# Kernel tuning notes

Measured on AMD Instinct MI355X. Metric: run time of the kernel, lower is better.

The kernel has to match this reference:

```python
import jax, jax.numpy as jnp
import numpy as np
from jax import lax

T, B, D = 1024, 32, 1024


def setup_inputs() -> dict:
    key = jax.random.key(0)
    k1, k2, k3, k4 = jax.random.split(key, 4)
    xav = (6.0 / (D + D)) ** 0.5  # xavier_uniform bound
    return {
        "x": jax.random.normal(k1, (T, B, D), dtype=jnp.float32),
        "h0": jnp.zeros((B, D), dtype=jnp.float32),
        "W_alpha": jax.random.uniform(k2, (D, D), minval=-xav, maxval=xav, dtype=jnp.float32),
        "d_alpha": jnp.full((D,), 0.1, dtype=jnp.float32),
        "b_alpha": jnp.full((D,), 2.0, dtype=jnp.float32),
        "W_x": jax.random.uniform(k3, (D, D), minval=-xav, maxval=xav, dtype=jnp.float32),
        "b_v": jnp.zeros((D,), dtype=jnp.float32),
    }


def reference(x, h0, W_alpha, d_alpha, b_alpha, W_x, b_v):
    # Precompute batched GEMMs once (x_t @ W.T), as in the original.
    alpha_x = jnp.einsum("tbd,ed->tbe", x, W_alpha)          # [T,B,D]
    v = jnp.tanh(jnp.einsum("tbd,ed->tbe", x, W_x) + b_v)    # [T,B,D]

    def step(h_prev, inp):
        ax_t, v_t = inp
        alpha = jax.nn.sigmoid(ax_t + d_alpha * h_prev + b_alpha)
        h_new = alpha * h_prev + (1.0 - alpha) * v_t
        out = h_new * h_new * jax.nn.sigmoid(h_new)  # h * silu(h)
        return h_new, (h_new, out)

    _, (hs, outs) = lax.scan(step, h0, (alpha_x, v))
    h = jnp.concatenate([h0[None], hs], axis=0)  # [T+1,B,D]
    return outs, h
```

## Files before the change

kernel.cpp:

```cpp
#include <hip/hip_runtime.h>
#include <hip/hip_bf16.h>
#include <stdint.h>

#define TT 1024
#define BB 32
#define DD 1024
#define MROWS (TT*BB)
#define NCOLS (2*DD)
#define KDIM  (DD)
#define SS (BB*DD)

typedef __attribute__((ext_vector_type(8))) short short8;
typedef __attribute__((ext_vector_type(4))) float f32x4;

__device__ __forceinline__ float bf2f(uint16_t u){
  union { uint32_t u; float f; } c; c.u = ((uint32_t)u) << 16; return c.f;
}
__device__ __forceinline__ uint16_t f2bf(float f){
  union { float f; uint32_t u; } c; c.f = f;
  uint32_t u = c.u;
  u += 0x7FFFu + ((u >> 16) & 1u);
  return (uint16_t)(u >> 16);
}
__device__ __forceinline__ float tanh_fast(float x){
  return 1.f - 2.f/(1.f + __expf(2.f*x));
}
__device__ __forceinline__ float sigmoid_fast(float x){
  return __builtin_amdgcn_rcpf(1.f + __expf(-x));
}

__global__ __launch_bounds__(256) void cvt_x_kernel(const float* __restrict__ x,
                                                    uint16_t* __restrict__ xb, int n4){
  int i = blockIdx.x * 256 + threadIdx.x;
  int stride = gridDim.x * 256;
  for (; i < n4; i += stride){
    float4 f = ((const float4*)x)[i];
    ushort4 o;
    o.x = f2bf(f.x); o.y = f2bf(f.y); o.z = f2bf(f.z); o.w = f2bf(f.w);
    ((ushort4*)xb)[i] = o;
  }
}

__global__ __launch_bounds__(256) void cvt_w_kernel(const float* __restrict__ Wa,
                                                    const float* __restrict__ Wx,
                                                    uint16_t* __restrict__ wc){
  int i = blockIdx.x * 256 + threadIdx.x;
  const int c    = i >> 8;
  const int col4 = i & 255;
  const int e = ((c >> 5) << 4) | (c & 15);
  const int s = (c >> 4) & 1;
  const float* src = (s ? Wx : Wa) + (size_t)e*DD + col4*4;
  float4 f = *(const float4*)src;
  ushort4 o;
  o.x = f2bf(f.x); o.y = f2bf(f.y); o.z = f2bf(f.z); o.w = f2bf(f.w);
  ((ushort4*)wc)[i] = o;
}

__global__ __launch_bounds__(512, 2) void gemm_dual(const uint16_t* __restrict__ xb,
                                                    const uint16_t* __restrict__ wc,
                                                    const float* __restrict__ bv,
                                                    uint32_t* __restrict__ av){
  __shared__ __align__(16) uint16_t lds[65536];
  char* ldsc = (char*)lds;

  const int tid  = threadIdx.x;
  const int lane = tid & 63;
  const int w    = tid >> 6;
  const int wm   = w >> 2;
  const int wn   = w & 3;
  const int fr   = lane & 15;
  const int fq   = lane >> 4;

  const int bid = blockIdx.x;
  const int bsw = (bid & 7) * 128 + (bid >> 3);
  const int bm  = (bsw >> 3) << 8;
  const int bn  = (bsw & 7) << 8;

  f32x4 acc[8][4] = {};

  const int srow = tid >> 3;
  const int soff = ((tid & 7) ^ (srow & 7)) * 8;

  #define STAGE(kt, q) { \
    const uint16_t* src_ = ((q) < 2) ? xb : wc; \
    const int gbase_ = ((q) < 2) ? bm : bn; \
    const int region_ = ((q) < 2) ? 0 : 65536; \
    const int rb0_ = ((q) & 1) * 128; \
    const int k0_ = (kt) * 64; \
    _Pragma("unroll") \
    for (int c_ = 0; c_ < 2; ++c_){ \
      const uint16_t* g_ = src_ + (size_t)(gbase_ + rb0_ + c_*64 + srow)*KDIM + k0_ + soff; \
      char* d_ = ldsc + region_ + ((kt) & 1)*32768 + (rb0_ + c_*64 + w*8)*128; \
      __builtin_amdgcn_global_load_lds((const __attribute__((address_space(1))) void*)g_, \
                                       (__attribute__((address_space(3))) void*)d_, 16, 0, 0); \
    } \
  }

  STAGE(0,0) STAGE(0,1) STAGE(0,2) STAGE(0,3)
  asm volatile("s_waitcnt vmcnt(0)" ::: "memory");
  __builtin_amdgcn_s_barrier();

  for (int t = 0; t < 16; ++t){
    const int nbuf = (t & 1) * 32768;
    const int aB0 = nbuf + (wm*128 + fr)*128;
    const int bB0 = 65536 + nbuf + (wn*64 + fr)*128;
    int aK[2], bK[2];
    #pragma unroll
    for (int kh = 0; kh < 2; ++kh){
      const int ps = ((kh*4 + fq) ^ (fr & 7)) * 16;
      aK[kh] = aB0 + ps;
      bK[kh] = bB0 + ps;
    }

    #define PHASE(q) { \
      short8 aF[4][2], bF[2][2]; \
      _Pragma("unroll") \
      for (int m = 0; m < 4; ++m) \
        _Pragma("unroll") \
        for (int kh = 0; kh < 2; ++kh) \
          aF[m][kh] = *(const short8*)(ldsc + aK[kh] + (((q)&1)*8192 + m*2048)); \
      _Pragma("unroll") \
      for (int n = 0; n < 2; ++n) \
        _Pragma("unroll") \
        for (int kh = 0; kh < 2; ++kh) \
          bF[n][kh] = *(const short8*)(ldsc + bK[kh] + (((q)>>1)*4096 + n*2048)); \
      if (t < 15) STAGE(t+1, q) \
      __builtin_amdgcn_s_barrier(); \
      asm volatile("s_waitcnt lgkmcnt(0)" ::: "memory"); \
      __builtin_amdgcn_sched_barrier(0); \
      __builtin_amdgcn_s_setprio(1); \
      _Pragma("unroll") \
      for (int m = 0; m < 4; ++m) \
        _Pragma("unroll") \
        for (int n = 0; n < 2; ++n) \
          _Pragma("unroll") \
          for (int kh = 0; kh < 2; ++kh) \
            acc[((q)&1)*4+m][((q)>>1)*2+n] = \
              __builtin_amdgcn_mfma_f32_16x16x32_bf16(aF[m][kh], bF[n][kh], \
                                                      acc[((q)&1)*4+m][((q)>>1)*2+n], 0, 0, 0); \
      __builtin_amdgcn_s_setprio(0); \
      if ((q) == 3) asm volatile("s_waitcnt vmcnt(0)" ::: "memory"); \
      __builtin_amdgcn_s_barrier(); \
    }

    PHASE(0) PHASE(1) PHASE(2) PHASE(3)
    #undef PHASE
  }
  #undef STAGE

  const int ebase = (bn + wn*64) >> 1;
  #pragma unroll
  for (int p = 0; p < 2; ++p){
    const int e = ebase + p*16 + fr;
    const float bvn = bv[e];
    #pragma unroll
    for (int m = 0; m < 8; ++m){
      #pragma unroll
      for (int j = 0; j < 4; ++j){
        const int row = bm + wm*128 + m*16 + fq*4 + j;
        const float a  = acc[m][2*p][j];
        const float vt = tanh_fast(acc[m][2*p+1][j] + bvn);
        const int tt = row >> 5, b = row & 31;
        av[(size_t)tt*SS + (size_t)b*DD + e] = (uint32_t)f2bf(a) | ((uint32_t)f2bf(vt) << 16);
      }
    }
  }
}

#define SCAN_STEP(u, tcur)                                        \
  {                                                               \
    const float a_ = bf2f((uint16_t)(u));                         \
    const float v_ = bf2f((uint16_t)((u) >> 16));                 \
    const float al_ = sigmoid_fast(a_ + da*h + ba);               \
    h = al_*(h - v_) + v_;                                        \
    const float sg_ = sigmoid_fast(h);                            \
    __builtin_nontemporal_store(h*h*sg_, &outs[(size_t)(tcur)*SS + idx]); \
    __builtin_nontemporal_store(h, &houts[(size_t)((tcur)+1)*SS + idx]);  \
  }

__global__ __launch_bounds__(64) void scan_kernel(const uint32_t* __restrict__ av,
                                                  const float* __restrict__ h0,
                                                  const float* __restrict__ d_alpha,
                                                  const float* __restrict__ b_alpha,
                                                  float* __restrict__ outs,
                                                  float* __restrict__ houts){
  const int idx = blockIdx.x * 64 + threadIdx.x;
  const int e = idx & (DD-1);
  const float da = d_alpha[e];
  const float ba = b_alpha[e];
  float h = h0[idx];
  __builtin_nontemporal_store(h, &houts[idx]);

  uint32_t bufA[32], bufB[32];
  #pragma unroll
  for (int j = 0; j < 32; ++j) bufA[j] = av[(size_t)j*SS + idx];

  for (int t0 = 0; t0 < TT; t0 += 64){
    #pragma unroll
    for (int j = 0; j < 32; ++j) bufB[j] = av[(size_t)(t0+32+j)*SS + idx];
    #pragma unroll
    for (int j = 0; j < 32; ++j) SCAN_STEP(bufA[j], t0 + j);
    if (t0 + 64 < TT){
      #pragma unroll
      for (int j = 0; j < 32; ++j) bufA[j] = av[(size_t)(t0+64+j)*SS + idx];
    }
    #pragma unroll
    for (int j = 0; j < 32; ++j) SCAN_STEP(bufB[j], t0 + 32 + j);
  }
}

extern "C" void kernel_launch(void* const* d_in, const int* in_sizes, int n_in,
                              void* d_out, int out_size, void* d_ws, size_t ws_size,
                              hipStream_t stream){
  const float* x  = (const float*)d_in[0];
  const float* h0 = (const float*)d_in[1];
  const float* Wa = (const float*)d_in[2];
  const float* da = (const float*)d_in[3];
  const float* ba = (const float*)d_in[4];
  const float* Wx = (const float*)d_in[5];
  const float* bv = (const float*)d_in[6];

  float* outs  = (float*)d_out;
  float* houts = outs + (size_t)TT*BB*DD;

  uint8_t* ws = (uint8_t*)d_ws;
  uint16_t* wcb = (uint16_t*)ws;
  uint16_t* xb  = (uint16_t*)(ws + (size_t)NCOLS*KDIM*2);
  uint32_t* av  = (uint32_t*)(ws + (size_t)NCOLS*KDIM*2 + (size_t)MROWS*KDIM*2);

  hipLaunchKernelGGL(cvt_w_kernel, dim3(2048), dim3(256), 0, stream, Wa, Wx, wcb);
  hipLaunchKernelGGL(cvt_x_kernel, dim3(2048), dim3(256), 0, stream, x, xb, MROWS*KDIM/4);
  hipLaunchKernelGGL(gemm_dual, dim3((NCOLS/256)*(MROWS/256)), dim3(512), 0, stream,
                     xb, wcb, bv, av);
  hipLaunchKernelGGL(scan_kernel, dim3(SS/64), dim3(64), 0, stream,
                     av, h0, da, ba, outs, houts);
}
```

Before: 273.2 us.

## Restructure GEMM to triple-buffered K=32 stages with prefetch two ahead

Changes the dual GEMM's LDS pipeline from double-buffered 64-wide K tiles to triple-buffered 32-wide K tiles, issuing global-to-LDS loads two iterations ahead and waiting with vmcnt(4) instead of draining fully. LDS use drops from 128KB to 96KB, and the swizzle and fragment layout are reworked to match. The aim is to hide global load latency more fully and cut stalls at barriers. The cost is twice as many loop iterations, each with barriers, and less MFMA work per synchronisation.

```diff
diff --git a/kernel.cpp b/kernel.cpp
--- a/kernel.cpp
+++ b/kernel.cpp
@@ -60,7 +60,7 @@
                                                     const uint16_t* __restrict__ wc,
                                                     const float* __restrict__ bv,
                                                     uint32_t* __restrict__ av){
-  __shared__ __align__(16) uint16_t lds[65536];
+  __shared__ __align__(16) uint16_t lds[49152];
   char* ldsc = (char*)lds;
 
   const int tid  = threadIdx.x;
@@ -78,91 +78,96 @@
 
   f32x4 acc[8][4] = {};
 
-  const int srow = tid >> 3;
-  const int soff = ((tid & 7) ^ (srow & 7)) * 8;
-
-  #define STAGE(kt, q) { \
-    const uint16_t* src_ = ((q) < 2) ? xb : wc; \
-    const int gbase_ = ((q) < 2) ? bm : bn; \
-    const int region_ = ((q) < 2) ? 0 : 65536; \
-    const int rb0_ = ((q) & 1) * 128; \
-    const int k0_ = (kt) * 64; \
-    _Pragma("unroll") \
-    for (int c_ = 0; c_ < 2; ++c_){ \
-      const uint16_t* g_ = src_ + (size_t)(gbase_ + rb0_ + c_*64 + srow)*KDIM + k0_ + soff; \
-      char* d_ = ldsc + region_ + ((kt) & 1)*32768 + (rb0_ + c_*64 + w*8)*128; \
-      __builtin_amdgcn_global_load_lds((const __attribute__((address_space(1))) void*)g_, \
-                                       (__attribute__((address_space(3))) void*)d_, 16, 0, 0); \
-    } \
-  }
-
-  STAGE(0,0) STAGE(0,1) STAGE(0,2) STAGE(0,3)
-  asm volatile("s_waitcnt vmcnt(0)" ::: "memory");
+  const int srow = tid >> 2;
+  const int soff = ((tid & 3) ^ ((tid >> 3) & 3)) * 8;
+
+  #define STAGE_UNIT(kt, bufb, u) { \
+    const uint16_t* s_ = ((u) < 2) ? xb : wc; \
+    const int gb_ = ((u) < 2) ? bm : bn; \
+    const int reg_ = ((u) < 2) ? 0 : 16384; \
+    const int rb_ = ((u) & 1) * 128; \
+    const uint16_t* g_ = s_ + (size_t)(gb_ + rb_ + srow)*KDIM + (kt)*32 + soff; \
+    char* d_ = ldsc + (bufb) + reg_ + rb_*64 + w*1024; \
+    __builtin_amdgcn_global_load_lds((const __attribute__((address_space(1))) void*)g_, \
+                                     (__attribute__((address_space(3))) void*)d_, 16, 0, 0); \
+  }
+
+  const int slotoff = (fq ^ ((fr >> 1) & 3)) * 16;
+  const int aoff0 = (wm*128 + fr)*64 + slotoff;
+  const int boff0 = 16384 + (wn*64 + fr)*64 + slotoff;
+
+  STAGE_UNIT(0, 0, 0) STAGE_UNIT(0, 0, 1) STAGE_UNIT(0, 0, 2) STAGE_UNIT(0, 0, 3)
+  STAGE_UNIT(1, 32768, 0) STAGE_UNIT(1, 32768, 1) STAGE_UNIT(1, 32768, 2) STAGE_UNIT(1, 32768, 3)
+  asm volatile("s_waitcnt vmcnt(4)" ::: "memory");
   __builtin_amdgcn_s_barrier();
 
-  for (int t = 0; t < 16; ++t){
-    const int nbuf = (t & 1) * 32768;
-    const int aB0 = nbuf + (wm*128 + fr)*128;
-    const int bB0 = 65536 + nbuf + (wn*64 + fr)*128;
-    int aK[2], bK[2];
-    #pragma unroll
-    for (int kh = 0; kh < 2; ++kh){
-      const int ps = ((kh*4 + fq) ^ (fr & 7)) * 16;
-      aK[kh] = aB0 + ps;
-      bK[kh] = bB0 + ps;
+  int bR = 0;
+  for (int t = 0; t < 32; ++t){
+    const int bRb = bR * 32768;
+    const int bW  = (bR == 0) ? 2 : (bR - 1);
+    const int bWb = bW * 32768;
+
+    short8 aF[4], bF[4];
+    #pragma unroll
+    for (int m = 0; m < 4; ++m)
+      aF[m] = *(const short8*)(ldsc + bRb + aoff0 + m*1024);
+    #pragma unroll
+    for (int n = 0; n < 4; ++n)
+      bF[n] = *(const short8*)(ldsc + bRb + boff0 + n*1024);
+    if (t < 30){ STAGE_UNIT(t+2, bWb, 0) STAGE_UNIT(t+2, bWb, 1) }
+    __builtin_amdgcn_s_barrier();
+    asm volatile("s_waitcnt lgkmcnt(0)" ::: "memory");
+    __builtin_amdgcn_sched_barrier(0);
+    __builtin_amdgcn_s_setprio(1);
+    #pragma unroll
+    for (int m = 0; m < 4; ++m)
+      #pragma unroll
+      for (int n = 0; n < 4; ++n)
+        acc[m][n] = __builtin_amdgcn_mfma_f32_16x16x32_bf16(aF[m], bF[n], acc[m][n], 0, 0, 0);
+    __builtin_amdgcn_s_setprio(0);
+    __builtin_amdgcn_s_barrier();
+
+    #pragma unroll
+    for (int m = 0; m < 4; ++m)
+      aF[m] = *(const short8*)(ldsc + bRb + aoff0 + 4096 + m*1024);
+    if (t < 30){ STAGE_UNIT(t+2, bWb, 2) STAGE_UNIT(t+2, bWb, 3) }
+    __builtin_amdgcn_s_barrier();
+    asm volatile("s_waitcnt lgkmcnt(0)" ::: "memory");
+    __builtin_amdgcn_sched_barrier(0);
+    __builtin_amdgcn_s_setprio(1);
+    #pragma unroll
+    for (int m = 0; m < 4; ++m)
+      #pragma unroll
+      for (int n = 0; n < 4; ++n)
+        acc[4+m][n] = __builtin_amdgcn_mfma_f32_16x16x32_bf16(aF[m], bF[n], acc[4+m][n], 0, 0, 0);
+    __builtin_amdgcn_s_setprio(0);
+    if (t < 30){
+      asm volatile("s_waitcnt vmcnt(4)" ::: "memory");
+    } else if (t == 30){
+      asm volatile("s_waitcnt vmcnt(0)" ::: "memory");
     }
-
-    #define PHASE(q) { \
-      short8 aF[4][2], bF[2][2]; \
-      _Pragma("unroll") \
-      for (int m = 0; m < 4; ++m) \
-        _Pragma("unroll") \
-        for (int kh = 0; kh < 2; ++kh) \
-          aF[m][kh] = *(const short8*)(ldsc + aK[kh] + (((q)&1)*8192 + m*2048)); \
-      _Pragma("unroll") \
-      for (int n = 0; n < 2; ++n) \
-        _Pragma("unroll") \
-        for (int kh = 0; kh < 2; ++kh) \
-          bF[n][kh] = *(const short8*)(ldsc + bK[kh] + (((q)>>1)*4096 + n*2048)); \
-      if (t < 15) STAGE(t+1, q) \
-      __builtin_amdgcn_s_barrier(); \
-      asm volatile("s_waitcnt lgkmcnt(0)" ::: "memory"); \
-      __builtin_amdgcn_sched_barrier(0); \
-      __builtin_amdgcn_s_setprio(1); \
-      _Pragma("unroll") \
-      for (int m = 0; m < 4; ++m) \
-        _Pragma("unroll") \
-        for (int n = 0; n < 2; ++n) \
-          _Pragma("unroll") \
-          for (int kh = 0; kh < 2; ++kh) \
-            acc[((q)&1)*4+m][((q)>>1)*2+n] = \
-              __builtin_amdgcn_mfma_f32_16x16x32_bf16(aF[m][kh], bF[n][kh], \
-                                                      acc[((q)&1)*4+m][((q)>>1)*2+n], 0, 0, 0); \
-      __builtin_amdgcn_s_setprio(0); \
-      if ((q) == 3) asm volatile("s_waitcnt vmcnt(0)" ::: "memory"); \
-      __builtin_amdgcn_s_barrier(); \
-    }
-
-    PHASE(0) PHASE(1) PHASE(2) PHASE(3)
-    #undef PHASE
-  }
-  #undef STAGE
+    __builtin_amdgcn_s_barrier();
+
+    bR = (bR == 2) ? 0 : (bR + 1);
+  }
+  #undef STAGE_UNIT
 
   const int ebase = (bn + wn*64) >> 1;
+  const float bvn0 = bv[ebase + fr];
+  const float bvn1 = bv[ebase + 16 + fr];
   #pragma unroll
-  for (int p = 0; p < 2; ++p){
-    const int e = ebase + p*16 + fr;
-    const float bvn = bv[e];
-    #pragma unroll
-    for (int m = 0; m < 8; ++m){
-      #pragma unroll
-      for (int j = 0; j < 4; ++j){
-        const int row = bm + wm*128 + m*16 + fq*4 + j;
-        const float a  = acc[m][2*p][j];
-        const float vt = tanh_fast(acc[m][2*p+1][j] + bvn);
-        const int tt = row >> 5, b = row & 31;
-        av[(size_t)tt*SS + (size_t)b*DD + e] = (uint32_t)f2bf(a) | ((uint32_t)f2bf(vt) << 16);
-      }
+  for (int m = 0; m < 8; ++m){
+    #pragma unroll
+    for (int j = 0; j < 4; ++j){
+      const int row = bm + wm*128 + m*16 + fq*4 + j;
+      const int tt = row >> 5, b = row & 31;
+      const size_t base = (size_t)tt*SS + (size_t)b*DD;
+      const float a0  = acc[m][0][j];
+      const float vt0 = tanh_fast(acc[m][1][j] + bvn0);
+      av[base + ebase + fr] = (uint32_t)f2bf(a0) | ((uint32_t)f2bf(vt0) << 16);
+      const float a1  = acc[m][2][j];
+      const float vt1 = tanh_fast(acc[m][3][j] + bvn1);
+      av[base + ebase + 16 + fr] = (uint32_t)f2bf(a1) | ((uint32_t)f2bf(vt1) << 16);
     }
   }
 }
```

Measured after the change: 266.3 us. 2.5% less time.
